# Kernel optimization log

Hardware: AMD Instinct MI355X
Metric: run time of the kernel (lower is better)

The kernel has to match this reference:

```python
import jax, jax.numpy as jnp
import numpy as np

B, TIN, IN, TRI, D, FFN, L, OUT = 8, 1040, 80, 128, 512, 2048, 8, 1024
H, DH, STRIDE, SEG, RC, LC, MAXMEM = 8, 64, 4, 16, 4, 32, 4
NEG = -1e8
SCALE = DH ** -0.5


def _layer_norm(x, g, b, eps=1e-5):
    m = jnp.mean(x, -1, keepdims=True)
    v = jnp.var(x, -1, keepdims=True)
    return (x - m) * jax.lax.rsqrt(v + eps) * g + b


def _build_attention_mask(U, nseg):
    # Faithful port of Emformer._gen_attention_mask; True = masked out.
    rct = RC * nseg
    mlen = nseg - 1
    rc_rows, q_rows, s_rows = [], [], []
    for i in range(nseg):
        rs, re = i * RC, i * RC + RC
        ss, se = max(i * SEG - LC, 0), min((i + 1) * SEG, U)
        ms = max(i - MAXMEM, 0)
        widths = [ms, i - ms, mlen - i, rs, RC, rct - re, ss, se - ss, U - se]

        def row(allowed):
            return np.concatenate([np.full(max(w, 0), j in allowed, dtype=bool)
                                   for j, w in enumerate(widths)])

        r = row({1, 4, 7})  # memory, own rc block, own (left-extended) segment
        rc_rows.append(np.tile(r, (RC, 1)))
        q_rows.append(np.tile(r, (min(SEG, U - i * SEG), 1)))
        s_rows.append(row({4, 7})[None])  # summary: rc block + segment only
    allow = np.concatenate([np.concatenate(rc_rows), np.concatenate(q_rows), np.concatenate(s_rows)])
    return jnp.asarray(~allow)


def _forward(input, lengths, w_in, ln_in_g, ln_in_b, wq, bq, wk, bk, wv, bv, wo, bo,
             ff_ln_g, ff_ln_b, w1, b1, w2, b2, ln_out_g, ln_out_b, w_out, b_out, lng, lnb):
    x = input @ w_in                                    # (B, TIN, TRI) input_linear (no bias)
    nb, t, _ = x.shape
    nf = t - t % STRIDE
    x = x[:, :nf].reshape(nb, nf // STRIDE, TRI * STRIDE)  # time reduction -> (B, Tr, D)
    lr = lengths // STRIDE
    x = jnp.transpose(x, (1, 0, 2))                     # (Tr, B, D) time-major like torch Emformer
    Tr = x.shape[0]
    U = Tr - RC                                         # utterance length (256)
    nseg = -(-U // SEG)
    utt = x[:U]
    # right-context blocks: hard-copied per segment (last block = trailing rc)
    starts = np.concatenate([np.arange(1, nseg) * SEG, [Tr - RC]])
    idx = (starts[:, None] + np.arange(RC)[None, :]).reshape(-1)
    rc = x[idx]                                         # (nseg*RC, B, D)
    Rt = rc.shape[0]
    Q = Rt + U + nseg                                   # rc + utterance + summary queries
    K = (nseg - 1) + Rt + U                             # mems + rc + utterance keys
    attn_mask = _build_attention_mask(U, nseg)          # (Q, K)
    mems0 = utt.reshape(nseg, SEG, nb, D).mean(1)[:-1]  # AvgPool1d(seg) on raw utterance, drop last
    # padding mask over keys (faithful to _gen_padding_mask)
    rcbl = Q - jnp.max(lr) - nseg
    klen = lr + (nseg - 1) + rcbl
    pad = jnp.arange(K)[None, :] >= klen[:, None]       # (B, K), True = masked

    def step(carry, p):
        utt, rc, mems = carry
        g1, be1, Wq, Bq, Wk, Bk, Wv, Bv, Wo, Bo, g2, be2, Wf1, Bf1, Wf2, Bf2, g3, be3 = p
        ln = _layer_norm(jnp.concatenate([rc, utt]), g1, be1)
        ln_rc, ln_utt = ln[:Rt], ln[Rt:]
        summary = ln_utt.reshape(nseg, SEG, nb, D).mean(1)       # (nseg, B, D)
        qin = jnp.concatenate([ln_rc, ln_utt, summary])          # (Q, B, D)
        kin = jnp.concatenate([mems, ln_rc, ln_utt])             # (K, B, D)
        q = (qin @ Wq + Bq).reshape(Q, nb, H, DH)
        k = (kin @ Wk + Bk).reshape(K, nb, H, DH)
        v = (kin @ Wv + Bv).reshape(K, nb, H, DH)
        w = jnp.einsum('qbhd,kbhd->bhqk', q * SCALE, k)
        w = jnp.where(attn_mask[None, None], NEG, w)
        w = jnp.where(pad[:, None, None, :], NEG, w)
        probs = jax.nn.softmax(w, axis=-1)
        att = jnp.einsum('bhqk,kbhd->qbhd', probs, v).reshape(Q, nb, D)
        out = att @ Wo + Bo
        rcu = out[:Rt + U]
        new_mems = jnp.tanh(out[Rt + U:])[:-1]                   # tanh_on_mem=True, drop last summary
        res = rcu + jnp.concatenate([rc, utt])                   # residual w/ pre-LN input
        h = _layer_norm(res, g2, be2)
        h = jax.nn.relu(h @ Wf1 + Bf1) @ Wf2 + Bf2               # pos_ff (pre-LN inside)
        res = res + h
        res = _layer_norm(res, g3, be3)
        return (res[Rt:], res[:Rt], new_mems), None

    xs = (ln_in_g, ln_in_b, wq, bq, wk, bk, wv, bv, wo, bo,
          ff_ln_g, ff_ln_b, w1, b1, w2, b2, ln_out_g, ln_out_b)
    (utt, rc, mems), _ = jax.lax.scan(step, (utt, rc, mems0), xs)
    y = jnp.transpose(utt, (1, 0, 2))                   # (B, U, D)
    y = _layer_norm(y @ w_out + b_out, lng, lnb)        # output_linear + LayerNorm
    return y, lr


def setup_inputs() -> dict:
    key = jax.random.key(0)
    ks = jax.random.split(key, 12)

    def w(k, shape, fan):
        return jax.random.normal(k, shape, jnp.float32) / np.sqrt(fan)

    return {
        "input": jax.random.normal(ks[0], (B, TIN, IN), jnp.float32),
        "lengths": jax.random.randint(ks[1], (B,), 256, 1025, jnp.int32),
        "w_in": w(ks[2], (IN, TRI), IN),
        "ln_in_g": jnp.ones((L, D), jnp.float32), "ln_in_b": jnp.zeros((L, D), jnp.float32),
        "wq": w(ks[3], (L, D, D), D), "bq": jnp.zeros((L, D), jnp.float32),
        "wk": w(ks[4], (L, D, D), D), "bk": jnp.zeros((L, D), jnp.float32),
        "wv": w(ks[5], (L, D, D), D), "bv": jnp.zeros((L, D), jnp.float32),
        "wo": w(ks[6], (L, D, D), D), "bo": jnp.zeros((L, D), jnp.float32),
        "ff_ln_g": jnp.ones((L, D), jnp.float32), "ff_ln_b": jnp.zeros((L, D), jnp.float32),
        "w1": w(ks[7], (L, D, FFN), D), "b1": jnp.zeros((L, FFN), jnp.float32),
        "w2": w(ks[8], (L, FFN, D), FFN), "b2": jnp.zeros((L, D), jnp.float32),
        "ln_out_g": jnp.ones((L, D), jnp.float32), "ln_out_b": jnp.zeros((L, D), jnp.float32),
        "w_out": w(ks[9], (D, OUT), D), "b_out": jnp.zeros((OUT,), jnp.float32),
        "lng": jnp.ones((OUT,), jnp.float32), "lnb": jnp.zeros((OUT,), jnp.float32),
    }


def reference(input, lengths, w_in, ln_in_g, ln_in_b, wq, bq, wk, bk, wv, bv, wo, bo,
              ff_ln_g, ff_ln_b, w1, b1, w2, b2, ln_out_g, ln_out_b, w_out, b_out, lng, lnb):
    return _forward(input, lengths, w_in, ln_in_g, ln_in_b, wq, bq, wk, bk, wv, bv, wo, bo,
                    ff_ln_g, ff_ln_b, w1, b1, w2, b2, ln_out_g, ln_out_b, w_out, b_out, lng, lnb)
```

## Files before the change

kernel.cpp:

```cpp
#include <hip/hip_runtime.h>
#include <math.h>

#define NB 8
#define D 512
#define H 8
#define DH 64
#define NSEG 16
#define RT 64
#define UU 256
#define QN 336
#define KN 335
#define SROWS 320
#define FFN_D 2048
#define LAYERS 8
#define OUTD 1024
#define TR 260
#define NEGV (-100000000.0f)
#define QSCALE 0.125f

typedef __attribute__((ext_vector_type(8))) short bf16x8;
typedef __attribute__((ext_vector_type(4))) float f32x4;

__device__ inline unsigned short f2bf(float f) {
    union { float f; unsigned int u; } v; v.f = f;
    unsigned int u = v.u;
    unsigned int r = (u + 0x7FFFu + ((u >> 16) & 1u)) >> 16;
    return (unsigned short)r;
}
__device__ inline float bf2f(unsigned short h) {
    union { unsigned int u; float f; } v; v.u = ((unsigned int)h) << 16;
    return v.f;
}

__device__ inline void async16(const void* g, void* l) {
    __builtin_amdgcn_global_load_lds((const __attribute__((address_space(1))) void*)g,
                                     (__attribute__((address_space(3))) void*)l, 16, 0, 0);
}

__global__ void lr_k(const int* __restrict__ lengths, int* __restrict__ lrw,
                     float* __restrict__ out_lr) {
    if (threadIdx.x == 0) {
        int mx = 0;
        for (int b = 0; b < NB; ++b) {
            int v = lengths[b] >> 2;
            lrw[b] = v;
            out_lr[b] = (float)v;
            if (v > mx) mx = v;
        }
        lrw[NB] = mx;
    }
}

__global__ __launch_bounds__(128) void inproj_k(const float* __restrict__ input,
                                                const float* __restrict__ w_in,
                                                float* __restrict__ XB) {
    __shared__ float wl[80 * 128];
    __shared__ float il[4 * 80];
    int tid = threadIdx.x;
    int t = blockIdx.x >> 3;
    int b = blockIdx.x & 7;
    for (int i = tid; i < 80 * 128; i += 128) wl[i] = w_in[i];
    const float* inp = input + ((size_t)b * 1040 + (size_t)t * 4) * 80;
    for (int i = tid; i < 320; i += 128) il[i] = inp[i];
    __syncthreads();
    float* xrow = XB + ((size_t)(t * NB + b)) * D;
#pragma unroll
    for (int c = 0; c < 4; ++c) {
        float acc = 0.f;
        for (int i = 0; i < 80; ++i) acc = fmaf(il[c * 80 + i], wl[i * 128 + tid], acc);
        xrow[c * 128 + tid] = acc;
    }
}

__global__ __launch_bounds__(256) void initstate_k(const float* __restrict__ XB,
                                                   float* __restrict__ S) {
    int r = blockIdx.x;
    int srow = r >> 3, b = r & 7;
    int src;
    if (srow < RT) {
        int i = srow >> 2, jj = srow & 3;
        src = (i < 15 ? (i + 1) * 16 : 256) + jj;
    } else {
        src = srow - RT;
    }
    const float* xr = XB + ((size_t)(src * NB + b)) * D;
    float* sr = S + (size_t)r * D;
    sr[threadIdx.x] = xr[threadIdx.x];
    sr[threadIdx.x + 256] = xr[threadIdx.x + 256];
}

__global__ __launch_bounds__(256) void mems0_k(const float* __restrict__ XB,
                                               unsigned short* __restrict__ MEMS) {
    int ib = blockIdx.x;
    int i = ib >> 3, b = ib & 7;
    for (int c = 0; c < 2; ++c) {
        int col = threadIdx.x + c * 256;
        float s = 0.f;
#pragma unroll
        for (int t = 0; t < 16; ++t) s += XB[((size_t)((i * 16 + t) * NB + b)) * D + col];
        MEMS[(size_t)ib * D + col] = f2bf(s * (1.f / 16.f));
    }
}

__global__ __launch_bounds__(256) void ln_k(const float* __restrict__ X,
                                            unsigned short* __restrict__ Y16,
                                            float* __restrict__ Yf,
                                            const float* __restrict__ g,
                                            const float* __restrict__ be, int dual) {
    int row = blockIdx.x;
    const float* x = X + (size_t)row * D;
    float v[2];
    float s = 0.f, ss = 0.f;
#pragma unroll
    for (int j = 0; j < 2; ++j) {
        v[j] = x[threadIdx.x + j * 256];
        s += v[j];
        ss = fmaf(v[j], v[j], ss);
    }
#pragma unroll
    for (int off = 32; off; off >>= 1) {
        s += __shfl_xor(s, off);
        ss += __shfl_xor(ss, off);
    }
    __shared__ float rs_[4], rss_[4];
    int w = threadIdx.x >> 6;
    if ((threadIdx.x & 63) == 0) {
        rs_[w] = s;
        rss_[w] = ss;
    }
    __syncthreads();
    s = rs_[0] + rs_[1] + rs_[2] + rs_[3];
    ss = rss_[0] + rss_[1] + rss_[2] + rss_[3];
    float mean = s * (1.f / D);
    float var = ss * (1.f / D) - mean * mean;
    float rstd = rsqrtf(var + 1e-5f);
#pragma unroll
    for (int j = 0; j < 2; ++j) {
        int col = threadIdx.x + j * 256;
        float y = (v[j] - mean) * rstd * g[col] + be[col];
        Y16[(size_t)row * D + col] = f2bf(y);
        if (dual) Yf[(size_t)row * D + col] = y;
    }
}

__global__ __launch_bounds__(256) void ln_res_k(const float* __restrict__ OUTB,
                                                float* __restrict__ SB,
                                                unsigned short* __restrict__ MEMS,
                                                unsigned short* __restrict__ Y16,
                                                const float* __restrict__ g,
                                                const float* __restrict__ be) {
    int row = blockIdx.x;
    if (row >= SROWS * NB) {
        int j = row - SROWS * NB;
#pragma unroll
        for (int c = 0; c < 2; ++c) {
            int col = threadIdx.x + c * 256;
            MEMS[(size_t)j * D + col] = f2bf(tanhf(OUTB[(size_t)row * D + col]));
        }
        return;
    }
    float v[2];
    float s = 0.f, ss = 0.f;
#pragma unroll
    for (int j = 0; j < 2; ++j) {
        int col = threadIdx.x + j * 256;
        float r = SB[(size_t)row * D + col] + OUTB[(size_t)row * D + col];
        SB[(size_t)row * D + col] = r;
        v[j] = r;
        s += r;
        ss = fmaf(r, r, ss);
    }
#pragma unroll
    for (int off = 32; off; off >>= 1) {
        s += __shfl_xor(s, off);
        ss += __shfl_xor(ss, off);
    }
    __shared__ float rs_[4], rss_[4];
    int w = threadIdx.x >> 6;
    if ((threadIdx.x & 63) == 0) {
        rs_[w] = s;
        rss_[w] = ss;
    }
    __syncthreads();
    s = rs_[0] + rs_[1] + rs_[2] + rs_[3];
    ss = rss_[0] + rss_[1] + rss_[2] + rss_[3];
    float mean = s * (1.f / D);
    float var = ss * (1.f / D) - mean * mean;
    float rstd = rsqrtf(var + 1e-5f);
#pragma unroll
    for (int j = 0; j < 2; ++j) {
        int col = threadIdx.x + j * 256;
        Y16[(size_t)row * D + col] = f2bf((v[j] - mean) * rstd * g[col] + be[col]);
    }
}

__global__ __launch_bounds__(256) void summary_k(const unsigned short* __restrict__ LN16,
                                                 unsigned short* __restrict__ SUM16) {
    int ib = blockIdx.x;
    int i = ib >> 3, b = ib & 7;
    for (int c = 0; c < 2; ++c) {
        int col = threadIdx.x + c * 256;
        float s = 0.f;
#pragma unroll
        for (int t = 0; t < 16; ++t)
            s += bf2f(LN16[((size_t)((RT + i * 16 + t) * NB + b)) * D + col]);
        SUM16[(size_t)ib * D + col] = f2bf(s * (1.f / 16.f));
    }
}

__device__ inline void conv_tile(float (*tile)[33], const float* __restrict__ src, int srcN,
                                 int k0, int sn0, unsigned short* __restrict__ dst, int dstK,
                                 int dn0) {
    int t = threadIdx.x;
    int r = t >> 3, c4 = (t & 7) * 4;
    float4 v = *(const float4*)&src[(size_t)(k0 + r) * srcN + sn0 + c4];
    tile[r][c4 + 0] = v.x;
    tile[r][c4 + 1] = v.y;
    tile[r][c4 + 2] = v.z;
    tile[r][c4 + 3] = v.w;
    __syncthreads();
    ushort4 o;
    o.x = f2bf(tile[c4 + 0][r]);
    o.y = f2bf(tile[c4 + 1][r]);
    o.z = f2bf(tile[c4 + 2][r]);
    o.w = f2bf(tile[c4 + 3][r]);
    *(ushort4*)&dst[(size_t)(dn0 + r) * dstK + k0 + c4] = o;
}

__global__ __launch_bounds__(256) void convw_all_k(const float* __restrict__ wq,
                                                   const float* __restrict__ wk,
                                                   const float* __restrict__ wv,
                                                   const float* __restrict__ wo,
                                                   const float* __restrict__ w1,
                                                   const float* __restrict__ w2,
                                                   const float* __restrict__ bq,
                                                   const float* __restrict__ bk,
                                                   const float* __restrict__ bv,
                                                   const float* __restrict__ w_out,
                                                   unsigned short* __restrict__ WQKV,
                                                   unsigned short* __restrict__ WO16,
                                                   unsigned short* __restrict__ W1T,
                                                   unsigned short* __restrict__ W2T,
                                                   unsigned short* __restrict__ WOUT16,
                                                   float* __restrict__ BQKV) {
    __shared__ float tile[32][33];
    int tb = blockIdx.x;
    if (tb >= LAYERS * 3072) {
        int t = tb - LAYERS * 3072;
        int n0 = (t % 32) * 32, k0 = (t / 32) * 32;
        conv_tile(tile, w_out, 1024, k0, n0, WOUT16, 512, n0);
        return;
    }
    int l = tb / 3072, t = tb % 3072;
    if (t == 0) {
        for (int i = threadIdx.x; i < 1536; i += 256)
            BQKV[l * 1536 + i] = i < 512 ? bq[l * 512 + i]
                                         : (i < 1024 ? bk[l * 512 + i - 512]
                                                     : bv[l * 512 + i - 1024]);
    }
    if (t < 768) {
        int tn = t % 48, tk = t / 48;
        int n0 = tn * 32, k0 = tk * 32;
        const float* src;
        int sn0;
        if (n0 < 512) { src = wq + (size_t)l * 262144; sn0 = n0; }
        else if (n0 < 1024) { src = wk + (size_t)l * 262144; sn0 = n0 - 512; }
        else { src = wv + (size_t)l * 262144; sn0 = n0 - 1024; }
        conv_tile(tile, src, 512, k0, sn0, WQKV + (size_t)l * 1536 * 512, 512, n0);
    } else if (t < 1024) {
        int tt = t - 768;
        int n0 = (tt % 16) * 32, k0 = (tt / 16) * 32;
        conv_tile(tile, wo + (size_t)l * 262144, 512, k0, n0, WO16 + (size_t)l * 512 * 512, 512,
                  n0);
    } else if (t < 2048) {
        int tt = t - 1024;
        int n0 = (tt % 64) * 32, k0 = (tt / 64) * 32;
        conv_tile(tile, w1 + (size_t)l * 1048576, 2048, k0, n0, W1T + (size_t)l * 2048 * 512, 512,
                  n0);
    } else {
        int tt = t - 2048;
        int n0 = (tt % 16) * 32, k0 = (tt / 16) * 32;
        conv_tile(tile, w2 + (size_t)l * 1048576, 512, k0, n0, W2T + (size_t)l * 512 * 2048, 2048,
                  n0);
    }
}

__global__ __launch_bounds__(256) void gemm16_k(const unsigned short* __restrict__ A,
                                                const unsigned short* __restrict__ BT,
                                                const float* __restrict__ bias,
                                                void* __restrict__ Cp, int M, int N, int K,
                                                int Kchunk, int flags) {
    __shared__ unsigned short As[64 * 64];
    __shared__ unsigned short Bs[64 * 64];
    int tid = threadIdx.x;
    int wave = tid >> 6, lane = tid & 63;
    int wm = wave >> 1, wn = wave & 1;
    int quad = lane >> 4, sub = lane & 15;
    int m0 = blockIdx.y * 64, n0 = blockIdx.x * 64;
    int kb = blockIdx.z * Kchunk, ke = kb + Kchunk;

    int s0 = wave * 128 + lane;
    int s1 = s0 + 64;
    int r0 = s0 >> 3, c0 = (s0 & 7) ^ (r0 & 7);
    int r1 = s1 >> 3, c1 = (s1 & 7) ^ (r1 & 7);
    const unsigned short* gA0 = A + (size_t)(m0 + r0) * K + c0 * 8 + kb;
    const unsigned short* gA1 = A + (size_t)(m0 + r1) * K + c1 * 8 + kb;
    const unsigned short* gB0 = BT + (size_t)(n0 + r0) * K + c0 * 8 + kb;
    const unsigned short* gB1 = BT + (size_t)(n0 + r1) * K + c1 * 8 + kb;
    unsigned short* lA0 = &As[(wave * 128) * 8];
    unsigned short* lA1 = &As[(wave * 128 + 64) * 8];
    unsigned short* lB0 = &Bs[(wave * 128) * 8];
    unsigned short* lB1 = &Bs[(wave * 128 + 64) * 8];

    int rowA0 = wm * 32 + sub, rowA1 = rowA0 + 16;
    int rowB0 = wn * 32 + sub, rowB1 = rowB0 + 16;

    f32x4 acc[2][2] = {};
    for (int k0 = 0; k0 < Kchunk; k0 += 64) {
        async16(gA0 + k0, lA0);
        async16(gA1 + k0, lA1);
        async16(gB0 + k0, lB0);
        async16(gB1 + k0, lB1);
        __syncthreads();
#pragma unroll
        for (int ks = 0; ks < 2; ++ks) {
            int cc = ks * 4 + quad;
            bf16x8 af0 = *(const bf16x8*)&As[rowA0 * 64 + ((cc ^ (rowA0 & 7)) * 8)];
            bf16x8 af1 = *(const bf16x8*)&As[rowA1 * 64 + ((cc ^ (rowA1 & 7)) * 8)];
            bf16x8 bf0 = *(const bf16x8*)&Bs[rowB0 * 64 + ((cc ^ (rowB0 & 7)) * 8)];
            bf16x8 bf1 = *(const bf16x8*)&Bs[rowB1 * 64 + ((cc ^ (rowB1 & 7)) * 8)];
            acc[0][0] = __builtin_amdgcn_mfma_f32_16x16x32_bf16(af0, bf0, acc[0][0], 0, 0, 0);
            acc[0][1] = __builtin_amdgcn_mfma_f32_16x16x32_bf16(af0, bf1, acc[0][1], 0, 0, 0);
            acc[1][0] = __builtin_amdgcn_mfma_f32_16x16x32_bf16(af1, bf0, acc[1][0], 0, 0, 0);
            acc[1][1] = __builtin_amdgcn_mfma_f32_16x16x32_bf16(af1, bf1, acc[1][1], 0, 0, 0);
        }
        __syncthreads();
    }
    (void)ke;

    bool relu = flags & 1, addc = flags & 2, obf = flags & 4, atom = flags & 8;
    bool addbias = !atom || blockIdx.z == 0;
    float* Cf = (float*)Cp;
    unsigned short* Ch = (unsigned short*)Cp;
#pragma unroll
    for (int mi = 0; mi < 2; ++mi) {
#pragma unroll
        for (int ni = 0; ni < 2; ++ni) {
#pragma unroll
            for (int r = 0; r < 4; ++r) {
                int row = m0 + wm * 32 + mi * 16 + quad * 4 + r;
                int col = n0 + wn * 32 + ni * 16 + sub;
                if (row < M) {
                    float v = acc[mi][ni][r] + (addbias ? bias[col] : 0.f);
                    if (relu) v = fmaxf(v, 0.f);
                    size_t idx = (size_t)row * N + col;
                    if (obf) {
                        Ch[idx] = f2bf(v);
                    } else if (atom) {
                        atomicAdd(&Cf[idx], v);
                    } else {
                        if (addc) v += Cf[idx];
                        Cf[idx] = v;
                    }
                }
            }
        }
    }
}

__global__ __launch_bounds__(256) void attn_k(const unsigned short* __restrict__ QKV,
                                              unsigned short* __restrict__ ATT,
                                              const int* __restrict__ lrw) {
    int tid = threadIdx.x;
    int qrow = blockIdx.x;
    int b = blockIdx.y;

    int i, is_sum;
    if (qrow < RT) {
        i = qrow >> 2;
        is_sum = 0;
    } else if (qrow < RT + UU) {
        i = (qrow - RT) >> 4;
        is_sum = 0;
    } else {
        i = qrow - (RT + UU);
        is_sum = 1;
    }
    int ms = (i > 4) ? (i - 4) : 0;
    int n_mem = is_sum ? 0 : (i - ms);
    int us = (i * 16 - 32 > 0) ? (i * 16 - 32) : 0;
    int ue = (i + 1) * 16;
    int total = n_mem + 4 + (ue - us);
    int klen = KN + lrw[b] - lrw[NB];

    __shared__ float qs[512];
    __shared__ float sc[H][64];
    __shared__ int kks[64];

    {
        const unsigned int* qrp =
            (const unsigned int*)&QKV[(size_t)(120 + qrow * NB + b) * 1536];
        unsigned int u = qrp[tid];
        qs[2 * tid] = __uint_as_float(u << 16) * QSCALE;
        qs[2 * tid + 1] = __uint_as_float(u & 0xFFFF0000u) * QSCALE;
    }
    if (tid < 64) {
        int kk = -1;
        if (tid < total) {
            if (tid < n_mem)
                kk = ms + tid;
            else if (tid < n_mem + 4)
                kk = 15 + i * 4 + (tid - n_mem);
            else
                kk = 79 + us + (tid - n_mem - 4);
        }
        kks[tid] = kk;
    }
    __syncthreads();

#pragma unroll
    for (int rep = 0; rep < 2; ++rep) {
        int p = rep * 256 + tid;
        int h = p >> 6, j = p & 63;
        int kk = kks[j];
        float s = NEGV;
        if (kk >= 0 && kk < klen) {
            const int4* kr = (const int4*)&QKV[(size_t)(kk * NB + b) * 1536 + 512 + h * DH];
            const float* qh = &qs[h * DH];
            float accd = 0.f;
#pragma unroll
            for (int c = 0; c < 8; ++c) {
                int4 kv = kr[c];
                const int uu[4] = {kv.x, kv.y, kv.z, kv.w};
#pragma unroll
                for (int jj = 0; jj < 4; ++jj) {
                    float lo = __uint_as_float(((unsigned)uu[jj]) << 16);
                    float hi = __uint_as_float(((unsigned)uu[jj]) & 0xFFFF0000u);
                    accd = fmaf(lo, qh[c * 8 + jj * 2], accd);
                    accd = fmaf(hi, qh[c * 8 + jj * 2 + 1], accd);
                }
            }
            s = accd;
        }
        sc[h][j] = s;
    }
    __syncthreads();

    {
        int wv = tid >> 6, lane = tid & 63;
#pragma unroll
        for (int hh = 0; hh < 2; ++hh) {
            int h = wv + hh * 4;
            float s = sc[h][lane];
            float m = s;
#pragma unroll
            for (int off = 32; off; off >>= 1) m = fmaxf(m, __shfl_xor(m, off));
            float p = __expf(s - m);
            float sum = p;
#pragma unroll
            for (int off = 32; off; off >>= 1) sum += __shfl_xor(sum, off);
            sc[h][lane] = p / sum;
        }
    }
    __syncthreads();

    {
        int h = tid >> 5;
        const float* ph = sc[h];
        float a0 = 0.f, a1 = 0.f;
        const unsigned short* vbase = QKV + (size_t)b * 1536 + 1024 + 2 * tid;
#pragma unroll 4
        for (int j = 0; j < total; ++j) {
            int kkj = kks[j];
            unsigned int u = *(const unsigned int*)&vbase[(size_t)kkj * (NB * 1536)];
            float p = ph[j];
            a0 = fmaf(p, __uint_as_float(u << 16), a0);
            a1 = fmaf(p, __uint_as_float(u & 0xFFFF0000u), a1);
        }
        unsigned int o = ((unsigned int)f2bf(a0)) | (((unsigned int)f2bf(a1)) << 16);
        *(unsigned int*)&ATT[(size_t)(qrow * NB + b) * D + 2 * tid] = o;
    }
}

__global__ __launch_bounds__(256) void final_ln_k(const float* __restrict__ Yb,
                                                  const float* __restrict__ g,
                                                  const float* __restrict__ be,
                                                  float* __restrict__ out) {
    int row = blockIdx.x;
    int u = row >> 3, b = row & 7;
    const float* x = Yb + (size_t)row * OUTD;
    float v[4];
    float s = 0.f, ss = 0.f;
#pragma unroll
    for (int j = 0; j < 4; ++j) {
        v[j] = x[threadIdx.x + j * 256];
        s += v[j];
        ss = fmaf(v[j], v[j], ss);
    }
#pragma unroll
    for (int off = 32; off; off >>= 1) {
        s += __shfl_xor(s, off);
        ss += __shfl_xor(ss, off);
    }
    __shared__ float rs_[4], rss_[4];
    int w = threadIdx.x >> 6;
    if ((threadIdx.x & 63) == 0) {
        rs_[w] = s;
        rss_[w] = ss;
    }
    __syncthreads();
    s = rs_[0] + rs_[1] + rs_[2] + rs_[3];
    ss = rss_[0] + rss_[1] + rss_[2] + rss_[3];
    float mean = s * (1.f / OUTD);
    float var = ss * (1.f / OUTD) - mean * mean;
    float rstd = rsqrtf(var + 1e-5f);
    float* o = out + ((size_t)(b * 256 + u)) * OUTD;
#pragma unroll
    for (int j = 0; j < 4; ++j) {
        int col = threadIdx.x + j * 256;
        o[col] = (v[j] - mean) * rstd * g[col] + be[col];
    }
}

extern "C" void kernel_launch(void* const* d_in, const int* in_sizes, int n_in, void* d_out,
                              int out_size, void* d_ws, size_t ws_size, hipStream_t stream) {
    (void)in_sizes;
    (void)n_in;
    (void)out_size;
    (void)ws_size;
    const float* input = (const float*)d_in[0];
    const int* lengths = (const int*)d_in[1];
    const float* w_in = (const float*)d_in[2];
    const float* ln_in_g = (const float*)d_in[3];
    const float* ln_in_b = (const float*)d_in[4];
    const float* wq = (const float*)d_in[5];
    const float* bq = (const float*)d_in[6];
    const float* wk = (const float*)d_in[7];
    const float* bk = (const float*)d_in[8];
    const float* wv = (const float*)d_in[9];
    const float* bv = (const float*)d_in[10];
    const float* wo = (const float*)d_in[11];
    const float* bo = (const float*)d_in[12];
    const float* ff_g = (const float*)d_in[13];
    const float* ff_b = (const float*)d_in[14];
    const float* w1 = (const float*)d_in[15];
    const float* b1 = (const float*)d_in[16];
    const float* w2 = (const float*)d_in[17];
    const float* b2 = (const float*)d_in[18];
    const float* lo_g = (const float*)d_in[19];
    const float* lo_b = (const float*)d_in[20];
    const float* w_out = (const float*)d_in[21];
    const float* b_out = (const float*)d_in[22];
    const float* lng = (const float*)d_in[23];
    const float* lnb = (const float*)d_in[24];
    float* out = (float*)d_out;

    char* wsc = (char*)d_ws;
    size_t off = 0;
    auto alloc = [&](size_t bytes) {
        char* p = wsc + off;
        off += (bytes + 255) & ~(size_t)255;
        return p;
    };
    unsigned short* ACT16 = (unsigned short*)alloc(2808ULL * 512 * 2);
    unsigned short* ATT16 = (unsigned short*)alloc(2688ULL * 512 * 2);
    unsigned short* HB16 = (unsigned short*)alloc(2560ULL * 2048 * 2);
    unsigned short* QKVB = (unsigned short*)alloc(2808ULL * 1536 * 2);
    float* SB = (float*)alloc(2560ULL * 512 * 4);
    unsigned short* WQKV16 = (unsigned short*)alloc(8ULL * 1536 * 512 * 2);
    unsigned short* WO16 = (unsigned short*)alloc(8ULL * 512 * 512 * 2);
    unsigned short* W1T = (unsigned short*)alloc(8ULL * 2048 * 512 * 2);
    unsigned short* W2T = (unsigned short*)alloc(8ULL * 512 * 2048 * 2);
    unsigned short* WOUT16 = (unsigned short*)alloc(1024ULL * 512 * 2);
    float* BQKV = (float*)alloc(8ULL * 1536 * 4);
    int* LRW = (int*)alloc(64);

    unsigned short* MEMS16 = ACT16;
    unsigned short* LNB16 = ACT16 + 120 * 512;
    unsigned short* SUMB16 = ACT16 + 2680 * 512;
    float* XB = (float*)QKVB;
    float* OUTB = (float*)QKVB;
    float* HBf = (float*)QKVB;

    lr_k<<<1, 64, 0, stream>>>(lengths, LRW, out + (size_t)NB * 256 * 1024);
    convw_all_k<<<LAYERS * 3072 + 512, 256, 0, stream>>>(wq, wk, wv, wo, w1, w2, bq, bk, bv,
                                                         w_out, WQKV16, WO16, W1T, W2T, WOUT16,
                                                         BQKV);
    inproj_k<<<TR * NB, 128, 0, stream>>>(input, w_in, XB);
    initstate_k<<<SROWS * NB, 256, 0, stream>>>(XB, SB);
    mems0_k<<<15 * NB, 256, 0, stream>>>(XB, MEMS16);

    for (int l = 0; l < LAYERS; ++l) {
        ln_k<<<SROWS * NB, 256, 0, stream>>>(SB, LNB16, SB, ln_in_g + l * D, ln_in_b + l * D, 0);
        summary_k<<<NSEG * NB, 256, 0, stream>>>(LNB16, SUMB16);
        gemm16_k<<<dim3(24, 44, 1), 256, 0, stream>>>(ACT16, WQKV16 + (size_t)l * 1536 * 512,
                                                      BQKV + l * 1536, QKVB, 2808, 1536, 512, 512,
                                                      4);
        attn_k<<<dim3(QN, NB), 256, 0, stream>>>(QKVB, ATT16, LRW);
        gemm16_k<<<dim3(8, 42, 1), 256, 0, stream>>>(ATT16, WO16 + (size_t)l * 512 * 512,
                                                     bo + l * D, OUTB, QN * NB, D, D, 512, 0);
        ln_res_k<<<(SROWS + 15) * NB, 256, 0, stream>>>(OUTB, SB, MEMS16, LNB16, ff_g + l * D,
                                                        ff_b + l * D);
        gemm16_k<<<dim3(32, 40, 1), 256, 0, stream>>>(LNB16, W1T + (size_t)l * 2048 * 512,
                                                      b1 + l * FFN_D, HB16, SROWS * NB, FFN_D,
                                                      512, 512, 1 | 4);
        gemm16_k<<<dim3(8, 40, 4), 256, 0, stream>>>(HB16, W2T + (size_t)l * 512 * 2048,
                                                     b2 + l * D, SB, SROWS * NB, D, FFN_D, 512,
                                                     8);
        ln_k<<<SROWS * NB, 256, 0, stream>>>(SB, LNB16, SB, lo_g + l * D, lo_b + l * D, 1);
    }
    gemm16_k<<<dim3(16, 32, 1), 256, 0, stream>>>(LNB16 + (size_t)RT * NB * D, WOUT16, b_out,
                                                  HBf, UU * NB, OUTD, 512, 512, 0);
    final_ln_k<<<UU * NB, 256, 0, stream>>>(HBf, lng, lnb, out);
}
```

Baseline: 1.113 ms.

## Add 128x128 MFMA GEMM tile for QKV/FFN and 64x64 weight-convert tiles

Adds a gemm128_k kernel with 128x128 output tiles, where each wave computes a 4x4 grid of 16x16 MFMA accumulators. The QKV, FFN1 and FFN2 projections now use it, which raises arithmetic intensity per LDS load and cuts global traffic compared with the 64x64 tiles. Row clamping is added so the M=2808 QKV GEMM, which is not a multiple of 128, reads in bounds, and the buffers are padded to match. The weight conversion kernel moves to 64x64 transposed tiles, so it launches a quarter as many blocks. The cost is more registers per thread, lower occupancy, and fewer blocks in flight on the smaller grids (for example 12x22 for QKV).

```diff
diff --git a/kernel.cpp b/kernel.cpp
--- a/kernel.cpp
+++ b/kernel.cpp
@@ -208,23 +208,34 @@
     }
 }
 
-__device__ inline void conv_tile(float (*tile)[33], const float* __restrict__ src, int srcN,
-                                 int k0, int sn0, unsigned short* __restrict__ dst, int dstK,
-                                 int dn0) {
+__device__ inline void conv_tile64(float (*tile)[65], const float* __restrict__ src, int srcN,
+                                   int k0, int sn0, unsigned short* __restrict__ dst, int dstK,
+                                   int dn0) {
     int t = threadIdx.x;
-    int r = t >> 3, c4 = (t & 7) * 4;
-    float4 v = *(const float4*)&src[(size_t)(k0 + r) * srcN + sn0 + c4];
-    tile[r][c4 + 0] = v.x;
-    tile[r][c4 + 1] = v.y;
-    tile[r][c4 + 2] = v.z;
-    tile[r][c4 + 3] = v.w;
-    __syncthreads();
-    ushort4 o;
-    o.x = f2bf(tile[c4 + 0][r]);
-    o.y = f2bf(tile[c4 + 1][r]);
-    o.z = f2bf(tile[c4 + 2][r]);
-    o.w = f2bf(tile[c4 + 3][r]);
-    *(ushort4*)&dst[(size_t)(dn0 + r) * dstK + k0 + c4] = o;
+#pragma unroll
+    for (int p = 0; p < 4; ++p) {
+        int r = p * 16 + (t >> 4);
+        int c = (t & 15) * 4;
+        *(float4*)&tile[r][c] = *(const float4*)&src[(size_t)(k0 + r) * srcN + sn0 + c];
+    }
+    __syncthreads();
+#pragma unroll
+    for (int p = 0; p < 2; ++p) {
+        int rn = p * 32 + (t >> 3);
+        int kc = (t & 7) * 8;
+        ushort4 o0, o1;
+        o0.x = f2bf(tile[kc + 0][rn]);
+        o0.y = f2bf(tile[kc + 1][rn]);
+        o0.z = f2bf(tile[kc + 2][rn]);
+        o0.w = f2bf(tile[kc + 3][rn]);
+        o1.x = f2bf(tile[kc + 4][rn]);
+        o1.y = f2bf(tile[kc + 5][rn]);
+        o1.z = f2bf(tile[kc + 6][rn]);
+        o1.w = f2bf(tile[kc + 7][rn]);
+        *(ushort4*)&dst[(size_t)(dn0 + rn) * dstK + k0 + kc] = o0;
+        *(ushort4*)&dst[(size_t)(dn0 + rn) * dstK + k0 + kc + 4] = o1;
+    }
+    __syncthreads();
 }
 
 __global__ __launch_bounds__(256) void convw_all_k(const float* __restrict__ wq,
@@ -243,45 +254,44 @@
                                                    unsigned short* __restrict__ W2T,
                                                    unsigned short* __restrict__ WOUT16,
                                                    float* __restrict__ BQKV) {
-    __shared__ float tile[32][33];
+    __shared__ float tile[64][65];
     int tb = blockIdx.x;
-    if (tb >= LAYERS * 3072) {
-        int t = tb - LAYERS * 3072;
-        int n0 = (t % 32) * 32, k0 = (t / 32) * 32;
-        conv_tile(tile, w_out, 1024, k0, n0, WOUT16, 512, n0);
+    if (tb >= LAYERS * 768) {
+        int t = tb - LAYERS * 768;
+        int n0 = (t % 16) * 64, k0 = (t / 16) * 64;
+        conv_tile64(tile, w_out, 1024, k0, n0, WOUT16, 512, n0);
         return;
     }
-    int l = tb / 3072, t = tb % 3072;
+    int l = tb / 768, t = tb % 768;
     if (t == 0) {
         for (int i = threadIdx.x; i < 1536; i += 256)
             BQKV[l * 1536 + i] = i < 512 ? bq[l * 512 + i]
                                          : (i < 1024 ? bk[l * 512 + i - 512]
                                                      : bv[l * 512 + i - 1024]);
     }
-    if (t < 768) {
-        int tn = t % 48, tk = t / 48;
-        int n0 = tn * 32, k0 = tk * 32;
+    if (t < 192) {
+        int n0 = (t % 24) * 64, k0 = (t / 24) * 64;
         const float* src;
         int sn0;
         if (n0 < 512) { src = wq + (size_t)l * 262144; sn0 = n0; }
         else if (n0 < 1024) { src = wk + (size_t)l * 262144; sn0 = n0 - 512; }
         else { src = wv + (size_t)l * 262144; sn0 = n0 - 1024; }
-        conv_tile(tile, src, 512, k0, sn0, WQKV + (size_t)l * 1536 * 512, 512, n0);
-    } else if (t < 1024) {
-        int tt = t - 768;
-        int n0 = (tt % 16) * 32, k0 = (tt / 16) * 32;
-        conv_tile(tile, wo + (size_t)l * 262144, 512, k0, n0, WO16 + (size_t)l * 512 * 512, 512,
-                  n0);
-    } else if (t < 2048) {
-        int tt = t - 1024;
-        int n0 = (tt % 64) * 32, k0 = (tt / 64) * 32;
-        conv_tile(tile, w1 + (size_t)l * 1048576, 2048, k0, n0, W1T + (size_t)l * 2048 * 512, 512,
-                  n0);
+        conv_tile64(tile, src, 512, k0, sn0, WQKV + (size_t)l * 1536 * 512, 512, n0);
+    } else if (t < 256) {
+        int tt = t - 192;
+        int n0 = (tt % 8) * 64, k0 = (tt / 8) * 64;
+        conv_tile64(tile, wo + (size_t)l * 262144, 512, k0, n0, WO16 + (size_t)l * 512 * 512, 512,
+                    n0);
+    } else if (t < 512) {
+        int tt = t - 256;
+        int n0 = (tt % 32) * 64, k0 = (tt / 32) * 64;
+        conv_tile64(tile, w1 + (size_t)l * 1048576, 2048, k0, n0, W1T + (size_t)l * 2048 * 512,
+                    512, n0);
     } else {
-        int tt = t - 2048;
-        int n0 = (tt % 16) * 32, k0 = (tt / 16) * 32;
-        conv_tile(tile, w2 + (size_t)l * 1048576, 512, k0, n0, W2T + (size_t)l * 512 * 2048, 2048,
-                  n0);
+        int tt = t - 512;
+        int n0 = (tt % 8) * 64, k0 = (tt / 8) * 64;
+        conv_tile64(tile, w2 + (size_t)l * 1048576, 512, k0, n0, W2T + (size_t)l * 512 * 2048,
+                    2048, n0);
     }
 }
 
@@ -297,14 +307,16 @@
     int wm = wave >> 1, wn = wave & 1;
     int quad = lane >> 4, sub = lane & 15;
     int m0 = blockIdx.y * 64, n0 = blockIdx.x * 64;
-    int kb = blockIdx.z * Kchunk, ke = kb + Kchunk;
+    int kb = blockIdx.z * Kchunk;
 
     int s0 = wave * 128 + lane;
     int s1 = s0 + 64;
     int r0 = s0 >> 3, c0 = (s0 & 7) ^ (r0 & 7);
     int r1 = s1 >> 3, c1 = (s1 & 7) ^ (r1 & 7);
-    const unsigned short* gA0 = A + (size_t)(m0 + r0) * K + c0 * 8 + kb;
-    const unsigned short* gA1 = A + (size_t)(m0 + r1) * K + c1 * 8 + kb;
+    int gra0 = m0 + r0; if (gra0 >= M) gra0 = M - 1;
+    int gra1 = m0 + r1; if (gra1 >= M) gra1 = M - 1;
+    const unsigned short* gA0 = A + (size_t)gra0 * K + c0 * 8 + kb;
+    const unsigned short* gA1 = A + (size_t)gra1 * K + c1 * 8 + kb;
     const unsigned short* gB0 = BT + (size_t)(n0 + r0) * K + c0 * 8 + kb;
     const unsigned short* gB1 = BT + (size_t)(n0 + r1) * K + c1 * 8 + kb;
     unsigned short* lA0 = &As[(wave * 128) * 8];
@@ -336,7 +348,6 @@
         }
         __syncthreads();
     }
-    (void)ke;
 
     bool relu = flags & 1, addc = flags & 2, obf = flags & 4, atom = flags & 8;
     bool addbias = !atom || blockIdx.z == 0;
@@ -350,6 +361,100 @@
             for (int r = 0; r < 4; ++r) {
                 int row = m0 + wm * 32 + mi * 16 + quad * 4 + r;
                 int col = n0 + wn * 32 + ni * 16 + sub;
+                if (row < M) {
+                    float v = acc[mi][ni][r] + (addbias ? bias[col] : 0.f);
+                    if (relu) v = fmaxf(v, 0.f);
+                    size_t idx = (size_t)row * N + col;
+                    if (obf) {
+                        Ch[idx] = f2bf(v);
+                    } else if (atom) {
+                        atomicAdd(&Cf[idx], v);
+                    } else {
+                        if (addc) v += Cf[idx];
+                        Cf[idx] = v;
+                    }
+                }
+            }
+        }
+    }
+}
+
+__global__ __launch_bounds__(256) void gemm128_k(const unsigned short* __restrict__ A,
+                                                 const unsigned short* __restrict__ BT,
+                                                 const float* __restrict__ bias,
+                                                 void* __restrict__ Cp, int M, int N, int K,
+                                                 int Kchunk, int flags) {
+    __shared__ unsigned short As[128 * 64];
+    __shared__ unsigned short Bs[128 * 64];
+    int tid = threadIdx.x;
+    int wave = tid >> 6, lane = tid & 63;
+    int wm = wave >> 1, wn = wave & 1;
+    int quad = lane >> 4, sub = lane & 15;
+    int m0 = blockIdx.y * 128, n0 = blockIdx.x * 128;
+    int kb = blockIdx.z * Kchunk;
+
+    const unsigned short* gA[4];
+    const unsigned short* gB[4];
+    unsigned short* lA[4];
+    unsigned short* lB[4];
+#pragma unroll
+    for (int q = 0; q < 4; ++q) {
+        int s = wave * 256 + q * 64 + lane;
+        int r = s >> 3, c = (s & 7) ^ (r & 7);
+        int gra = m0 + r;
+        if (gra >= M) gra = M - 1;
+        gA[q] = A + (size_t)gra * K + c * 8 + kb;
+        gB[q] = BT + (size_t)(n0 + r) * K + c * 8 + kb;
+        lA[q] = &As[(wave * 256 + q * 64) * 8];
+        lB[q] = &Bs[(wave * 256 + q * 64) * 8];
+    }
+
+    int rowA[4], rowB[4];
+#pragma unroll
+    for (int mi = 0; mi < 4; ++mi) rowA[mi] = wm * 64 + mi * 16 + sub;
+#pragma unroll
+    for (int ni = 0; ni < 4; ++ni) rowB[ni] = wn * 64 + ni * 16 + sub;
+
+    f32x4 acc[4][4] = {};
+    for (int k0 = 0; k0 < Kchunk; k0 += 64) {
+#pragma unroll
+        for (int q = 0; q < 4; ++q) {
+            async16(gA[q] + k0, lA[q]);
+            async16(gB[q] + k0, lB[q]);
+        }
+        __syncthreads();
+#pragma unroll
+        for (int ks = 0; ks < 2; ++ks) {
+            int cc = ks * 4 + quad;
+            bf16x8 af[4], bf[4];
+#pragma unroll
+            for (int mi = 0; mi < 4; ++mi)
+                af[mi] = *(const bf16x8*)&As[rowA[mi] * 64 + ((cc ^ (rowA[mi] & 7)) * 8)];
+#pragma unroll
+            for (int ni = 0; ni < 4; ++ni)
+                bf[ni] = *(const bf16x8*)&Bs[rowB[ni] * 64 + ((cc ^ (rowB[ni] & 7)) * 8)];
+#pragma unroll
+            for (int mi = 0; mi < 4; ++mi)
+#pragma unroll
+                for (int ni = 0; ni < 4; ++ni)
+                    acc[mi][ni] = __builtin_amdgcn_mfma_f32_16x16x32_bf16(af[mi], bf[ni],
+                                                                          acc[mi][ni], 0, 0, 0);
+        }
+        __syncthreads();
+    }
+
+    bool relu = flags & 1, addc = flags & 2, obf = flags & 4, atom = flags & 8;
+    bool addbias = !atom || blockIdx.z == 0;
+    float* Cf = (float*)Cp;
+    unsigned short* Ch = (unsigned short*)Cp;
+#pragma unroll
+    for (int mi = 0; mi < 4; ++mi) {
+#pragma unroll
+        for (int ni = 0; ni < 4; ++ni) {
+#pragma unroll
+            for (int r = 0; r < 4; ++r) {
+                int row = m0 + wm * 64 + mi * 16 + quad * 4 + r;
+                int col = n0 + wn * 64 + ni * 16 + sub;
                 if (row < M) {
                     float v = acc[mi][ni][r] + (addbias ? bias[col] : 0.f);
                     if (relu) v = fmaxf(v, 0.f);
@@ -562,10 +667,10 @@
         off += (bytes + 255) & ~(size_t)255;
         return p;
     };
-    unsigned short* ACT16 = (unsigned short*)alloc(2808ULL * 512 * 2);
+    unsigned short* ACT16 = (unsigned short*)alloc(2816ULL * 512 * 2);
     unsigned short* ATT16 = (unsigned short*)alloc(2688ULL * 512 * 2);
     unsigned short* HB16 = (unsigned short*)alloc(2560ULL * 2048 * 2);
-    unsigned short* QKVB = (unsigned short*)alloc(2808ULL * 1536 * 2);
+    unsigned short* QKVB = (unsigned short*)alloc(2816ULL * 1536 * 2);
     float* SB = (float*)alloc(2560ULL * 512 * 4);
     unsigned short* WQKV16 = (unsigned short*)alloc(8ULL * 1536 * 512 * 2);
     unsigned short* WO16 = (unsigned short*)alloc(8ULL * 512 * 512 * 2);
@@ -583,9 +688,9 @@
     float* HBf = (float*)QKVB;
 
     lr_k<<<1, 64, 0, stream>>>(lengths, LRW, out + (size_t)NB * 256 * 1024);
-    convw_all_k<<<LAYERS * 3072 + 512, 256, 0, stream>>>(wq, wk, wv, wo, w1, w2, bq, bk, bv,
-                                                         w_out, WQKV16, WO16, W1T, W2T, WOUT16,
-                                                         BQKV);
+    convw_all_k<<<LAYERS * 768 + 128, 256, 0, stream>>>(wq, wk, wv, wo, w1, w2, bq, bk, bv,
+                                                        w_out, WQKV16, WO16, W1T, W2T, WOUT16,
+                                                        BQKV);
     inproj_k<<<TR * NB, 128, 0, stream>>>(input, w_in, XB);
     initstate_k<<<SROWS * NB, 256, 0, stream>>>(XB, SB);
     mems0_k<<<15 * NB, 256, 0, stream>>>(XB, MEMS16);
@@ -593,20 +698,20 @@
     for (int l = 0; l < LAYERS; ++l) {
         ln_k<<<SROWS * NB, 256, 0, stream>>>(SB, LNB16, SB, ln_in_g + l * D, ln_in_b + l * D, 0);
         summary_k<<<NSEG * NB, 256, 0, stream>>>(LNB16, SUMB16);
-        gemm16_k<<<dim3(24, 44, 1), 256, 0, stream>>>(ACT16, WQKV16 + (size_t)l * 1536 * 512,
-                                                      BQKV + l * 1536, QKVB, 2808, 1536, 512, 512,
-                                                      4);
+        gemm128_k<<<dim3(12, 22, 1), 256, 0, stream>>>(ACT16, WQKV16 + (size_t)l * 1536 * 512,
+                                                       BQKV + l * 1536, QKVB, 2808, 1536, 512,
+                                                       512, 4);
         attn_k<<<dim3(QN, NB), 256, 0, stream>>>(QKVB, ATT16, LRW);
         gemm16_k<<<dim3(8, 42, 1), 256, 0, stream>>>(ATT16, WO16 + (size_t)l * 512 * 512,
                                                      bo + l * D, OUTB, QN * NB, D, D, 512, 0);
         ln_res_k<<<(SROWS + 15) * NB, 256, 0, stream>>>(OUTB, SB, MEMS16, LNB16, ff_g + l * D,
                                                         ff_b + l * D);
-        gemm16_k<<<dim3(32, 40, 1), 256, 0, stream>>>(LNB16, W1T + (size_t)l * 2048 * 512,
-                                                      b1 + l * FFN_D, HB16, SROWS * NB, FFN_D,
-                                                      512, 512, 1 | 4);
-        gemm16_k<<<dim3(8, 40, 4), 256, 0, stream>>>(HB16, W2T + (size_t)l * 512 * 2048,
-                                                     b2 + l * D, SB, SROWS * NB, D, FFN_D, 512,
-                                                     8);
+        gemm128_k<<<dim3(16, 20, 1), 256, 0, stream>>>(LNB16, W1T + (size_t)l * 2048 * 512,
+                                                       b1 + l * FFN_D, HB16, SROWS * NB, FFN_D,
+                                                       512, 512, 1 | 4);
+        gemm128_k<<<dim3(4, 20, 4), 256, 0, stream>>>(HB16, W2T + (size_t)l * 512 * 2048,
+                                                      b2 + l * D, SB, SROWS * NB, D, FFN_D, 512,
+                                                      8);
         ln_k<<<SROWS * NB, 256, 0, stream>>>(SB, LNB16, SB, lo_g + l * D, lo_b + l * D, 1);
     }
     gemm16_k<<<dim3(16, 32, 1), 256, 0, stream>>>(LNB16 + (size_t)RT * NB * D, WOUT16, b_out,
```

Measured after the change: 1.383 ms. 1.24x slower.
